# Kernel tuning notes

Hardware: AMD Instinct MI355X
Metric: run time of the kernel (lower is better)

## Reference

```python
import jax, jax.numpy as jnp
import numpy as np

B, N = 8192, 128          # batch, num intruders
D_OWN, D_GRID, D_INTR = 16, 512, 20
H, OUT = 128, 4


def setup_inputs() -> dict:
    key = jax.random.key(0)
    ks = jax.random.split(key, 12)
    rn = lambda k, shape, s=1.0: jax.random.normal(k, shape, jnp.float32) * s
    return {
        "state0": rn(ks[0], (B, D_OWN)),
        "state1": rn(ks[1], (B, D_GRID)),
        "state2": rn(ks[2], (B, N, D_INTR)),
        "W_own": rn(ks[3], (D_OWN, H), 0.1), "b_own": jnp.zeros((H,), jnp.float32),
        "W_intr": rn(ks[4], (D_INTR, H), 0.1), "b_intr": jnp.zeros((H,), jnp.float32),
        "W_grid": rn(ks[5], (D_GRID, H), 0.05), "b_grid": jnp.zeros((H,), jnp.float32),
        "Wq": rn(ks[6], (H, H), 0.08),
        "Wk": rn(ks[7], (H, H), 0.08),
        "Wv": rn(ks[8], (H, H), 0.08),
        "W1": rn(ks[9], (3 * H, H), 0.05), "b1": jnp.zeros((H,), jnp.float32),
        "W2": rn(ks[10], (H, OUT), 0.1), "b2": jnp.zeros((OUT,), jnp.float32),
    }


def reference(state0, state1, state2, W_own, b_own, W_intr, b_intr,
              W_grid, b_grid, Wq, Wk, Wv, W1, b1, W2, b2):
    own_e = jax.nn.relu(state0 @ W_own + b_own)            # [B,H]
    x_e = jax.nn.relu(state2 @ W_intr + b_intr)            # [B,N,H]
    q = own_e @ Wq                                         # [B,H]
    k = x_e @ Wk                                           # [B,N,H]
    v = x_e @ Wv                                           # [B,N,H]
    # mask = state2.mean(axis=2, keepdim=True).bool()  (nonzero test)
    mask = jnp.mean(state2, axis=2, keepdims=True) != 0    # [B,N,1]
    score = jnp.einsum('bnh,bh->bn', k, q)[..., None]      # bmm(k, q.unsqueeze(2)) -> [B,N,1]
    score = jnp.where(mask, score, -jnp.inf)
    alpha = jax.nn.softmax(score / np.float32(np.sqrt(H)), axis=1)
    alpha = jnp.where(mask, alpha, 0.0)
    v_att = jnp.sum(v * alpha, axis=1)                     # [B,H]
    own_grid = jax.nn.relu(state1 @ W_grid + b_grid)       # [B,H]
    concat = jnp.concatenate([own_e, v_att, own_grid], axis=1)  # [B,3H]
    out = (concat @ W1 + b1) @ W2 + b2                     # action_out_SAC
    mean = out
    log_std = jnp.clip(out, -20.0, 2.0)
    return mean, log_std
```

## Files before the change

kernel.cpp:

```cpp
#include <hip/hip_runtime.h>

typedef unsigned short ushort_t;
typedef __attribute__((ext_vector_type(8))) short bf16x8;
typedef __attribute__((ext_vector_type(4))) float f32x4;

__device__ __forceinline__ float bflo(unsigned u) { return __uint_as_float(u << 16); }
__device__ __forceinline__ float bfhi(unsigned u) { return __uint_as_float(u & 0xffff0000u); }
__device__ __forceinline__ float bfu(ushort_t s)  { return __uint_as_float((unsigned)s << 16); }
__device__ __forceinline__ ushort_t f2bf(float f) {
    unsigned u = __float_as_uint(f);
    u = u + 0x7fffu + ((u >> 16) & 1u);
    return (ushort_t)(u >> 16);
}
__device__ __forceinline__ void unpack8(uint4 v, float* f) {
    f[0]=bflo(v.x); f[1]=bfhi(v.x); f[2]=bflo(v.y); f[3]=bfhi(v.y);
    f[4]=bflo(v.z); f[5]=bfhi(v.z); f[6]=bflo(v.w); f[7]=bfhi(v.w);
}

__device__ __forceinline__ float load1(const void* p, size_t i, int f32) {
    return f32 ? ((const float*)p)[i] : bfu(((const ushort_t*)p)[i]);
}
__device__ __forceinline__ void load8(const void* p, size_t i, int f32, float* f) {
    if (f32) {
        const float4 a = *(const float4*)((const float*)p + i);
        const float4 b = *(const float4*)((const float*)p + i + 4);
        f[0]=a.x; f[1]=a.y; f[2]=a.z; f[3]=a.w;
        f[4]=b.x; f[5]=b.y; f[6]=b.z; f[7]=b.w;
    } else {
        unpack8(*(const uint4*)((const ushort_t*)p + i), f);
    }
}
__device__ __forceinline__ void load4(const void* p, size_t i, int f32, float* f) {
    if (f32) {
        const float4 a = *(const float4*)((const float*)p + i);
        f[0]=a.x; f[1]=a.y; f[2]=a.z; f[3]=a.w;
    } else {
        const uint2 u = *(const uint2*)((const ushort_t*)p + i);
        f[0]=bflo(u.x); f[1]=bfhi(u.x); f[2]=bflo(u.y); f[3]=bfhi(u.y);
    }
}

__device__ __forceinline__ int detect_f32(const ushort_t* s1h) {
    const int ln = threadIdx.x & 63;
    float v = fmaxf(fabsf(bfu(s1h[ln])), fabsf(bfu(s1h[ln + 64])));
    bool big = !(v <= 1e6f);
    return __ballot(big) != 0ull;
}

#define B_TOT 8192

__device__ __attribute__((aligned(16))) float    g_M[128 * 128];
__device__ __attribute__((aligned(16))) float    g_Wc1[384 * 4];
__device__ __attribute__((aligned(16))) float    g_Wv2[128 * 4];
__device__ __attribute__((aligned(16))) float    g_bc[4];
__device__ __attribute__((aligned(16))) float    g_t[B_TOT * 128];
__device__ __attribute__((aligned(16))) float    g_ogc[B_TOT * 4];
__device__ __attribute__((aligned(16))) ushort_t g_oe[B_TOT * 128];

__global__ __launch_bounds__(128) void k_pre(
    const void* __restrict__ Wq, const void* __restrict__ Wk,
    const void* __restrict__ Wv, const void* __restrict__ W1,
    const void* __restrict__ b1, const void* __restrict__ W2,
    const void* __restrict__ b2, const ushort_t* __restrict__ s1h)
{
    __shared__ float wq_sh[128];
    __shared__ float w2_sh[512];
    __shared__ float wc1_mid[512];
    __shared__ float redc[128][4];
    const int tid = threadIdx.x;
    const int bx = blockIdx.x;
    const int f32 = detect_f32(s1h);

    if (bx < 128) {
        wq_sh[tid] = load1(Wq, bx*128 + tid, f32);
        __syncthreads();
        float acc = 0.f;
        #pragma unroll
        for (int c = 0; c < 16; ++c) {
            float f[8]; load8(Wk, (size_t)tid*128 + c*8, f32, f);
            #pragma unroll
            for (int j = 0; j < 8; ++j) acc = fmaf(wq_sh[c*8+j], f[j], acc);
        }
        g_M[bx*128 + tid] = acc;
    } else {
        const int rbase = (bx == 128) ? 0 : ((bx == 129) ? 128 : 256);
        for (int i = tid; i < 512; i += 128) w2_sh[i] = load1(W2, i, f32);
        __syncthreads();

        const int r = rbase + tid;
        float a[4] = {0.f, 0.f, 0.f, 0.f};
        #pragma unroll
        for (int c = 0; c < 16; ++c) {
            float f[8]; load8(W1, (size_t)r*128 + c*8, f32, f);
            #pragma unroll
            for (int j = 0; j < 8; ++j) {
                const int p = c*8 + j;
                #pragma unroll
                for (int q = 0; q < 4; ++q) a[q] = fmaf(f[j], w2_sh[p*4+q], a[q]);
            }
        }
        #pragma unroll
        for (int q = 0; q < 4; ++q) g_Wc1[r*4+q] = a[q];

        if (bx == 129) {
            #pragma unroll
            for (int q = 0; q < 4; ++q) wc1_mid[tid*4+q] = a[q];
            __syncthreads();
            float v[4] = {0.f, 0.f, 0.f, 0.f};
            #pragma unroll
            for (int c = 0; c < 16; ++c) {
                float f[8]; load8(Wv, (size_t)tid*128 + c*8, f32, f);
                #pragma unroll
                for (int j = 0; j < 8; ++j) {
                    const int i2 = c*8 + j;
                    #pragma unroll
                    for (int q = 0; q < 4; ++q) v[q] = fmaf(f[j], wc1_mid[i2*4+q], v[q]);
                }
            }
            #pragma unroll
            for (int q = 0; q < 4; ++q) g_Wv2[tid*4+q] = v[q];

            const float bv = load1(b1, tid, f32);
            #pragma unroll
            for (int q = 0; q < 4; ++q) redc[tid][q] = bv * w2_sh[tid*4+q];
            __syncthreads();
            for (int s = 64; s > 0; s >>= 1) {
                if (tid < s) {
                    #pragma unroll
                    for (int q = 0; q < 4; ++q) redc[tid][q] += redc[tid+s][q];
                }
                __syncthreads();
            }
            if (tid < 4) g_bc[tid] = redc[0][tid] + load1(b2, tid, f32);
        }
    }
}

__global__ __launch_bounds__(256) void k_ownt(
    const void* __restrict__ state0, const void* __restrict__ W_own,
    const void* __restrict__ b_own, const ushort_t* __restrict__ s1h)
{
    __shared__ float s0sh[16*16];
    __shared__ float wosh[16*128];
    __shared__ float bosh[128];
    __shared__ float oesh[16*129];
    __shared__ float Mt[32][128];
    const int tid = threadIdx.x;
    const int b0 = blockIdx.x * 16;
    const int f32 = detect_f32(s1h);

    if (tid < 32) {
        float f[8]; load8(state0, (size_t)b0*16 + tid*8, f32, f);
        #pragma unroll
        for (int j = 0; j < 8; ++j) s0sh[tid*8 + j] = f[j];
    }
    {
        float f[8]; load8(W_own, (size_t)tid*8, f32, f);
        #pragma unroll
        for (int j = 0; j < 8; ++j) wosh[tid*8 + j] = f[j];
    }
    if (tid < 128) bosh[tid] = load1(b_own, tid, f32);
    __syncthreads();

    #pragma unroll
    for (int kk = 0; kk < 8; ++kk) {
        const int idx = tid + kk*256;
        const int bi = idx >> 7, h = idx & 127;
        float acc = bosh[h];
        #pragma unroll
        for (int d = 0; d < 16; ++d) acc = fmaf(s0sh[bi*16+d], wosh[d*128+h], acc);
        acc = fmaxf(acc, 0.f);
        oesh[bi*129 + h] = acc;
        g_oe[(size_t)(b0+bi)*128 + h] = f2bf(acc);
    }

    const int bi0 = (tid >> 5) * 2;
    const int h0  = (tid & 31) * 4;
    float t00=0.f,t01=0.f,t02=0.f,t03=0.f,t10=0.f,t11=0.f,t12=0.f,t13=0.f;
    for (int kt = 0; kt < 128; kt += 32) {
        __syncthreads();
        #pragma unroll
        for (int c = 0; c < 4; ++c) {
            const int i = tid + c*256;
            const int kk = i >> 5;
            const int hh = (i & 31) * 4;
            *(float4*)&Mt[kk][hh] = *(const float4*)&g_M[(size_t)(kt+kk)*128 + hh];
        }
        __syncthreads();
        #pragma unroll
        for (int k = 0; k < 32; ++k) {
            const float4 mv = *(const float4*)&Mt[k][h0];
            const float a0 = oesh[(bi0+0)*129 + kt + k];
            const float a1 = oesh[(bi0+1)*129 + kt + k];
            t00=fmaf(a0,mv.x,t00); t01=fmaf(a0,mv.y,t01); t02=fmaf(a0,mv.z,t02); t03=fmaf(a0,mv.w,t03);
            t10=fmaf(a1,mv.x,t10); t11=fmaf(a1,mv.y,t11); t12=fmaf(a1,mv.z,t12); t13=fmaf(a1,mv.w,t13);
        }
    }
    *(float4*)&g_t[(size_t)(b0+bi0+0)*128 + h0] = make_float4(t00,t01,t02,t03);
    *(float4*)&g_t[(size_t)(b0+bi0+1)*128 + h0] = make_float4(t10,t11,t12,t13);
}

__global__ __launch_bounds__(256) void k_grid(
    const void* __restrict__ state1, const void* __restrict__ W_grid,
    const void* __restrict__ b_grid)
{
    __shared__ float s1T[32][18];
    __shared__ float wg[32][128];
    __shared__ float part[32][16][4];
    const int tid = threadIdx.x;
    const int b0 = blockIdx.x * 16;
    const int f32 = detect_f32((const ushort_t*)state1);

    const int bq = tid & 7;
    const int hq = tid >> 3;
    float a00=0.f,a01=0.f,a02=0.f,a03=0.f;
    float a10=0.f,a11=0.f,a12=0.f,a13=0.f;

    for (int kt = 0; kt < 512; kt += 32) {
        if (kt) __syncthreads();
        if (tid < 128) {
            const int bb = tid >> 3;
            const int kk = (tid & 7) * 4;
            float f[4];
            load4(state1, (size_t)(b0 + bb)*512 + kt + kk, f32, f);
            #pragma unroll
            for (int j = 0; j < 4; ++j) s1T[kk + j][bb] = f[j];
        }
        {
            #pragma unroll
            for (int c = 0; c < 4; ++c) {
                const int i = tid + c*256;
                const int kk = i >> 5;
                const int hh = (i & 31) * 4;
                float f[4];
                load4(W_grid, (size_t)(kt + kk)*128 + hh, f32, f);
                *(float4*)&wg[kk][hh] = make_float4(f[0], f[1], f[2], f[3]);
            }
        }
        __syncthreads();
        #pragma unroll 8
        for (int k = 0; k < 32; ++k) {
            const float x0 = s1T[k][bq*2 + 0];
            const float x1 = s1T[k][bq*2 + 1];
            const float4 w = *(const float4*)&wg[k][hq*4];
            a00=fmaf(x0,w.x,a00); a01=fmaf(x0,w.y,a01); a02=fmaf(x0,w.z,a02); a03=fmaf(x0,w.w,a03);
            a10=fmaf(x1,w.x,a10); a11=fmaf(x1,w.y,a11); a12=fmaf(x1,w.z,a12); a13=fmaf(x1,w.w,a13);
        }
    }

    float accs[2][4] = {{a00,a01,a02,a03},{a10,a11,a12,a13}};
    float pr[2][4] = {{0,0,0,0},{0,0,0,0}};
    #pragma unroll
    for (int jh = 0; jh < 4; ++jh) {
        const int h = hq*4 + jh;
        const float bg = load1(b_grid, h, f32);
        const float4 wc = *(const float4*)&g_Wc1[(256 + h)*4];
        #pragma unroll
        for (int ib = 0; ib < 2; ++ib) {
            const float og = fmaxf(accs[ib][jh] + bg, 0.f);
            pr[ib][0] = fmaf(og, wc.x, pr[ib][0]);
            pr[ib][1] = fmaf(og, wc.y, pr[ib][1]);
            pr[ib][2] = fmaf(og, wc.z, pr[ib][2]);
            pr[ib][3] = fmaf(og, wc.w, pr[ib][3]);
        }
    }
    __syncthreads();
    #pragma unroll
    for (int j = 0; j < 4; ++j) {
        part[hq][bq*2+0][j] = pr[0][j];
        part[hq][bq*2+1][j] = pr[1][j];
    }
    __syncthreads();
    if (tid < 64) {
        const int bb = tid >> 2, j = tid & 3;
        float s = 0.f;
        #pragma unroll
        for (int q = 0; q < 32; ++q) s += part[q][bb][j];
        g_ogc[(size_t)(b0 + bb)*4 + j] = s;
    }
}

__global__ __launch_bounds__(256) void k_main(
    const void* __restrict__ state2, const void* __restrict__ W_intr,
    const void* __restrict__ b_intr, const ushort_t* __restrict__ s1h,
    void* __restrict__ out_raw)
{
    __shared__ __attribute__((aligned(16))) ushort_t wib[128 * 40];
    const int tid = threadIdx.x;
    const int f32 = detect_f32(s1h);

    #pragma unroll
    for (int c = 0; c < 10; ++c) {
        const int idx = c*256 + tid;
        const int d = idx >> 7, h = idx & 127;
        wib[h*40 + d] = f32 ? f2bf(((const float*)W_intr)[idx])
                            : ((const ushort_t*)W_intr)[idx];
    }
    if (tid < 128) {
        #pragma unroll
        for (int k = 20; k < 32; ++k) wib[tid*40 + k] = 0;
    }
    __syncthreads();

    const int wv = tid >> 6, ln = tid & 63, lq = ln >> 4, lc = ln & 15;
    const int b = blockIdx.x * 4 + wv;

    float bi_r[8], t_r[8];
    #pragma unroll
    for (int th = 0; th < 8; ++th) {
        bi_r[th] = load1(b_intr, th*16 + lc, f32);
        t_r[th]  = g_t[(size_t)b*128 + th*16 + lc] * 0.08838834764831845f;
    }

    bf16x8 A[8];
    unsigned msk[8];
    if (!f32) {
        const ushort_t* s2 = (const ushort_t*)state2;
        #pragma unroll
        for (int i = 0; i < 8; ++i) {
            const size_t rb = ((size_t)b*128 + i*16 + lc)*20 + lq*8;
            uint2 p0 = make_uint2(0u, 0u), p1 = make_uint2(0u, 0u);
            if (lq < 2)       { p0 = *(const uint2*)(s2 + rb); p1 = *(const uint2*)(s2 + rb + 4); }
            else if (lq == 2) { p0 = *(const uint2*)(s2 + rb); }
            union { bf16x8 v; uint2 u[2]; } cv;
            cv.u[0] = p0; cv.u[1] = p1;
            A[i] = cv.v;
            float s = bflo(p0.x)+bfhi(p0.x)+bflo(p0.y)+bfhi(p0.y)
                    + bflo(p1.x)+bfhi(p1.x)+bflo(p1.y)+bfhi(p1.y);
            s += __shfl_xor(s, 16);
            s += __shfl_xor(s, 32);
            msk[i] = (unsigned)(__ballot(s != 0.f) & 0xffffull);
        }
    } else {
        const float* s2 = (const float*)state2;
        #pragma unroll
        for (int i = 0; i < 8; ++i) {
            const size_t rb = ((size_t)b*128 + i*16 + lc)*20 + lq*8;
            float f[8] = {0.f,0.f,0.f,0.f,0.f,0.f,0.f,0.f};
            if (lq < 2) {
                const float4 a4 = *(const float4*)(s2 + rb);
                const float4 b4 = *(const float4*)(s2 + rb + 4);
                f[0]=a4.x; f[1]=a4.y; f[2]=a4.z; f[3]=a4.w;
                f[4]=b4.x; f[5]=b4.y; f[6]=b4.z; f[7]=b4.w;
            } else if (lq == 2) {
                const float4 a4 = *(const float4*)(s2 + rb);
                f[0]=a4.x; f[1]=a4.y; f[2]=a4.z; f[3]=a4.w;
            }
            union { bf16x8 v; ushort_t h[8]; } cv;
            float s = 0.f;
            #pragma unroll
            for (int j = 0; j < 8; ++j) { cv.h[j] = f2bf(f[j]); s += f[j]; }
            A[i] = cv.v;
            s += __shfl_xor(s, 16);
            s += __shfl_xor(s, 32);
            msk[i] = (unsigned)(__ballot(s != 0.f) & 0xffffull);
        }
    }

    const f32x4 zf = {0.f, 0.f, 0.f, 0.f};

    float sc[8][4];
    #pragma unroll
    for (int i = 0; i < 8; ++i)
        #pragma unroll
        for (int r = 0; r < 4; ++r) sc[i][r] = 0.f;

    #pragma unroll
    for (int th = 0; th < 8; ++th) {
        const bf16x8 Bv = *(const bf16x8*)&wib[(th*16 + lc)*40 + lq*8];
        #pragma unroll
        for (int i = 0; i < 8; ++i) {
            const f32x4 acc = __builtin_amdgcn_mfma_f32_16x16x32_bf16(A[i], Bv, zf, 0, 0, 0);
            #pragma unroll
            for (int r = 0; r < 4; ++r)
                sc[i][r] = fmaf(fmaxf(acc[r] + bi_r[th], 0.f), t_r[th], sc[i][r]);
        }
    }
    #pragma unroll
    for (int off = 1; off < 16; off <<= 1)
        #pragma unroll
        for (int i = 0; i < 8; ++i)
            #pragma unroll
            for (int r = 0; r < 4; ++r)
                sc[i][r] += __shfl_xor(sc[i][r], off);

    float m = -1e30f;
    #pragma unroll
    for (int i = 0; i < 8; ++i)
        #pragma unroll
        for (int r = 0; r < 4; ++r)
            if ((msk[i] >> (lq*4 + r)) & 1) m = fmaxf(m, sc[i][r]);
    m = fmaxf(m, __shfl_xor(m, 16));
    m = fmaxf(m, __shfl_xor(m, 32));

    float den = 0.f;
    #pragma unroll
    for (int i = 0; i < 8; ++i)
        #pragma unroll
        for (int r = 0; r < 4; ++r) {
            float e = 0.f;
            if ((msk[i] >> (lq*4 + r)) & 1) e = __expf(fmaxf(sc[i][r] - m, -80.f));
            sc[i][r] = e;
            den += e;
        }
    den += __shfl_xor(den, 16);
    den += __shfl_xor(den, 32);
    const float rden = (den > 0.f) ? (1.f / den) : 0.f;
    #pragma unroll
    for (int i = 0; i < 8; ++i)
        #pragma unroll
        for (int r = 0; r < 4; ++r) sc[i][r] *= rden;

    float o4[4] = {0.f, 0.f, 0.f, 0.f};
    #pragma unroll
    for (int th = 0; th < 8; ++th) {
        const bf16x8 Bv = *(const bf16x8*)&wib[(th*16 + lc)*40 + lq*8];
        float up = 0.f;
        #pragma unroll
        for (int i = 0; i < 8; ++i) {
            const f32x4 acc = __builtin_amdgcn_mfma_f32_16x16x32_bf16(A[i], Bv, zf, 0, 0, 0);
            #pragma unroll
            for (int r = 0; r < 4; ++r)
                up = fmaf(sc[i][r], fmaxf(acc[r] + bi_r[th], 0.f), up);
        }
        const float4 w2 = *(const float4*)&g_Wv2[(th*16 + lc)*4];
        o4[0] = fmaf(up, w2.x, o4[0]);
        o4[1] = fmaf(up, w2.y, o4[1]);
        o4[2] = fmaf(up, w2.z, o4[2]);
        o4[3] = fmaf(up, w2.w, o4[3]);
    }

    {
        const float oe0 = bfu(g_oe[(size_t)b*128 + ln]);
        const float oe1 = bfu(g_oe[(size_t)b*128 + 64 + ln]);
        const float4 wA = *(const float4*)&g_Wc1[ln*4];
        const float4 wB = *(const float4*)&g_Wc1[(64 + ln)*4];
        o4[0] += oe0*wA.x + oe1*wB.x;
        o4[1] += oe0*wA.y + oe1*wB.y;
        o4[2] += oe0*wA.z + oe1*wB.z;
        o4[3] += oe0*wA.w + oe1*wB.w;
    }

    #pragma unroll
    for (int off = 1; off < 64; off <<= 1)
        #pragma unroll
        for (int q = 0; q < 4; ++q)
            o4[q] += __shfl_xor(o4[q], off);

    if (ln == 0) {
        const float4 og = *(const float4*)&g_ogc[(size_t)b*4];
        const float v0 = g_bc[0] + og.x + o4[0];
        const float v1 = g_bc[1] + og.y + o4[1];
        const float v2 = g_bc[2] + og.z + o4[2];
        const float v3 = g_bc[3] + og.w + o4[3];
        const float l0 = fminf(fmaxf(v0, -20.f), 2.f);
        const float l1 = fminf(fmaxf(v1, -20.f), 2.f);
        const float l2 = fminf(fmaxf(v2, -20.f), 2.f);
        const float l3 = fminf(fmaxf(v3, -20.f), 2.f);
        if (f32) {
            float* of = (float*)out_raw;
            *(float4*)&of[(size_t)b*4] = make_float4(v0, v1, v2, v3);
            *(float4*)&of[((size_t)B_TOT + b)*4] = make_float4(l0, l1, l2, l3);
        } else {
            ushort_t* os = (ushort_t*)out_raw;
            uint2 mw, lw;
            mw.x = (unsigned)f2bf(v0) | ((unsigned)f2bf(v1) << 16);
            mw.y = (unsigned)f2bf(v2) | ((unsigned)f2bf(v3) << 16);
            lw.x = (unsigned)f2bf(l0) | ((unsigned)f2bf(l1) << 16);
            lw.y = (unsigned)f2bf(l2) | ((unsigned)f2bf(l3) << 16);
            *(uint2*)&os[(size_t)b*4] = mw;
            *(uint2*)&os[((size_t)B_TOT + b)*4] = lw;
        }
    }
}

extern "C" void kernel_launch(void* const* d_in, const int* in_sizes, int n_in,
                              void* d_out, int out_size, void* d_ws, size_t ws_size,
                              hipStream_t stream)
{
    (void)in_sizes; (void)n_in; (void)out_size; (void)d_ws; (void)ws_size;
    const void* state0 = d_in[0];
    const void* state1 = d_in[1];
    const void* state2 = d_in[2];
    const void* W_own  = d_in[3];
    const void* b_own  = d_in[4];
    const void* W_intr = d_in[5];
    const void* b_intr = d_in[6];
    const void* W_grid = d_in[7];
    const void* b_grid = d_in[8];
    const void* Wq     = d_in[9];
    const void* Wk     = d_in[10];
    const void* Wv     = d_in[11];
    const void* W1     = d_in[12];
    const void* b1     = d_in[13];
    const void* W2     = d_in[14];
    const void* b2     = d_in[15];
    const ushort_t* s1h = (const ushort_t*)state1;

    k_pre  <<<dim3(131),  dim3(128), 0, stream>>>(Wq, Wk, Wv, W1, b1, W2, b2, s1h);
    k_ownt <<<dim3(512),  dim3(256), 0, stream>>>(state0, W_own, b_own, s1h);
    k_grid <<<dim3(512),  dim3(256), 0, stream>>>(state1, W_grid, b_grid);
    k_main <<<dim3(2048), dim3(256), 0, stream>>>(state2, W_intr, b_intr, s1h, d_out);
}
```

Measured before the change: 291.8 us.

## Fold bias, mask and softmax scaling into MFMA and exp2 in attention kernel

Folds the intruder bias into the MFMA by appending a constant-one input column and a bias row in the LDS weight tile. The mask row sums are computed with an extra MFMA against a ones vector instead of shuffle-and-ballot reductions. The log2(e) factor is pre-scaled into the query so the softmax can use raw exp2, and normalisation is deferred to the four outputs instead of all scores. State2 loads are also hoisted ahead of the weight staging and barrier to overlap global latency. This removes per-element bias adds, masking branches and reductions, at the cost of the bias being rounded to bf16 and slightly different masking semantics.

```diff
diff --git a/kernel.cpp b/kernel.cpp
--- a/kernel.cpp
+++ b/kernel.cpp
@@ -289,6 +289,50 @@
     const int tid = threadIdx.x;
     const int f32 = detect_f32(s1h);
 
+    const int wv = tid >> 6, ln = tid & 63, lq = ln >> 4, lc = ln & 15;
+    const int b = blockIdx.x * 4 + wv;
+
+    bf16x8 A[8];
+    if (!f32) {
+        const ushort_t* base = (const ushort_t*)state2 + ((size_t)b*128 + lc)*20 + lq*8;
+        #pragma unroll
+        for (int i = 0; i < 8; ++i) {
+            uint2 p0 = make_uint2(0u, 0u), p1 = make_uint2(0u, 0u);
+            if (lq < 2)       { p0 = *(const uint2*)(base + i*320); p1 = *(const uint2*)(base + i*320 + 4); }
+            else if (lq == 2) { p0 = *(const uint2*)(base + i*320); p1.x = 0x00003f80u; }
+            union { bf16x8 v; uint2 u[2]; } cv;
+            cv.u[0] = p0; cv.u[1] = p1;
+            A[i] = cv.v;
+        }
+    } else {
+        const float* base = (const float*)state2 + ((size_t)b*128 + lc)*20 + lq*8;
+        #pragma unroll
+        for (int i = 0; i < 8; ++i) {
+            float f[8] = {0.f,0.f,0.f,0.f,0.f,0.f,0.f,0.f};
+            if (lq < 2) {
+                const float4 a4 = *(const float4*)(base + i*320);
+                const float4 b4 = *(const float4*)(base + i*320 + 4);
+                f[0]=a4.x; f[1]=a4.y; f[2]=a4.z; f[3]=a4.w;
+                f[4]=b4.x; f[5]=b4.y; f[6]=b4.z; f[7]=b4.w;
+            } else if (lq == 2) {
+                const float4 a4 = *(const float4*)(base + i*320);
+                f[0]=a4.x; f[1]=a4.y; f[2]=a4.z; f[3]=a4.w;
+                f[4]=1.0f;
+            }
+            union { bf16x8 v; ushort_t h[8]; } cv;
+            #pragma unroll
+            for (int j = 0; j < 8; ++j) cv.h[j] = f2bf(f[j]);
+            A[i] = cv.v;
+        }
+    }
+
+    float t_r[8];
+    {
+        const float* tb = &g_t[(size_t)b*128 + lc];
+        #pragma unroll
+        for (int th = 0; th < 8; ++th) t_r[th] = tb[th*16] * 0.12751743f;
+    }
+
     #pragma unroll
     for (int c = 0; c < 10; ++c) {
         const int idx = c*256 + tid;
@@ -297,67 +341,25 @@
                             : ((const ushort_t*)W_intr)[idx];
     }
     if (tid < 128) {
-        #pragma unroll
-        for (int k = 20; k < 32; ++k) wib[tid*40 + k] = 0;
+        wib[tid*40 + 20] = f32 ? f2bf(((const float*)b_intr)[tid])
+                               : ((const ushort_t*)b_intr)[tid];
+        #pragma unroll
+        for (int k = 21; k < 32; ++k) wib[tid*40 + k] = 0;
     }
     __syncthreads();
 
-    const int wv = tid >> 6, ln = tid & 63, lq = ln >> 4, lc = ln & 15;
-    const int b = blockIdx.x * 4 + wv;
-
-    float bi_r[8], t_r[8];
-    #pragma unroll
-    for (int th = 0; th < 8; ++th) {
-        bi_r[th] = load1(b_intr, th*16 + lc, f32);
-        t_r[th]  = g_t[(size_t)b*128 + th*16 + lc] * 0.08838834764831845f;
-    }
-
-    bf16x8 A[8];
-    unsigned msk[8];
-    if (!f32) {
-        const ushort_t* s2 = (const ushort_t*)state2;
-        #pragma unroll
-        for (int i = 0; i < 8; ++i) {
-            const size_t rb = ((size_t)b*128 + i*16 + lc)*20 + lq*8;
-            uint2 p0 = make_uint2(0u, 0u), p1 = make_uint2(0u, 0u);
-            if (lq < 2)       { p0 = *(const uint2*)(s2 + rb); p1 = *(const uint2*)(s2 + rb + 4); }
-            else if (lq == 2) { p0 = *(const uint2*)(s2 + rb); }
-            union { bf16x8 v; uint2 u[2]; } cv;
-            cv.u[0] = p0; cv.u[1] = p1;
-            A[i] = cv.v;
-            float s = bflo(p0.x)+bfhi(p0.x)+bflo(p0.y)+bfhi(p0.y)
-                    + bflo(p1.x)+bfhi(p1.x)+bflo(p1.y)+bfhi(p1.y);
-            s += __shfl_xor(s, 16);
-            s += __shfl_xor(s, 32);
-            msk[i] = (unsigned)(__ballot(s != 0.f) & 0xffffull);
-        }
-    } else {
-        const float* s2 = (const float*)state2;
-        #pragma unroll
-        for (int i = 0; i < 8; ++i) {
-            const size_t rb = ((size_t)b*128 + i*16 + lc)*20 + lq*8;
-            float f[8] = {0.f,0.f,0.f,0.f,0.f,0.f,0.f,0.f};
-            if (lq < 2) {
-                const float4 a4 = *(const float4*)(s2 + rb);
-                const float4 b4 = *(const float4*)(s2 + rb + 4);
-                f[0]=a4.x; f[1]=a4.y; f[2]=a4.z; f[3]=a4.w;
-                f[4]=b4.x; f[5]=b4.y; f[6]=b4.z; f[7]=b4.w;
-            } else if (lq == 2) {
-                const float4 a4 = *(const float4*)(s2 + rb);
-                f[0]=a4.x; f[1]=a4.y; f[2]=a4.z; f[3]=a4.w;
-            }
-            union { bf16x8 v; ushort_t h[8]; } cv;
-            float s = 0.f;
-            #pragma unroll
-            for (int j = 0; j < 8; ++j) { cv.h[j] = f2bf(f[j]); s += f[j]; }
-            A[i] = cv.v;
-            s += __shfl_xor(s, 16);
-            s += __shfl_xor(s, 32);
-            msk[i] = (unsigned)(__ballot(s != 0.f) & 0xffffull);
-        }
-    }
+    union { bf16x8 v; unsigned u[4]; } bo;
+    bo.u[0] = (lq <= 2) ? 0x3f803f80u : 0u;
+    bo.u[1] = (lq <= 2) ? 0x3f803f80u : 0u;
+    bo.u[2] = (lq <= 1) ? 0x3f803f80u : 0u;
+    bo.u[3] = (lq <= 1) ? 0x3f803f80u : 0u;
 
     const f32x4 zf = {0.f, 0.f, 0.f, 0.f};
+
+    f32x4 ms[8];
+    #pragma unroll
+    for (int i = 0; i < 8; ++i)
+        ms[i] = __builtin_amdgcn_mfma_f32_16x16x32_bf16(A[i], bo.v, zf, 0, 0, 0);
 
     float sc[8][4];
     #pragma unroll
@@ -373,7 +375,7 @@
             const f32x4 acc = __builtin_amdgcn_mfma_f32_16x16x32_bf16(A[i], Bv, zf, 0, 0, 0);
             #pragma unroll
             for (int r = 0; r < 4; ++r)
-                sc[i][r] = fmaf(fmaxf(acc[r] + bi_r[th], 0.f), t_r[th], sc[i][r]);
+                sc[i][r] = fmaf(fmaxf(acc[r], 0.f), t_r[th], sc[i][r]);
         }
     }
     #pragma unroll
@@ -384,12 +386,16 @@
             for (int r = 0; r < 4; ++r)
                 sc[i][r] += __shfl_xor(sc[i][r], off);
 
+    #pragma unroll
+    for (int i = 0; i < 8; ++i)
+        #pragma unroll
+        for (int r = 0; r < 4; ++r)
+            sc[i][r] = (ms[i][r] != 0.f) ? sc[i][r] : -1e30f;
+
     float m = -1e30f;
     #pragma unroll
     for (int i = 0; i < 8; ++i)
-        #pragma unroll
-        for (int r = 0; r < 4; ++r)
-            if ((msk[i] >> (lq*4 + r)) & 1) m = fmaxf(m, sc[i][r]);
+        m = fmaxf(m, fmaxf(fmaxf(sc[i][0], sc[i][1]), fmaxf(sc[i][2], sc[i][3])));
     m = fmaxf(m, __shfl_xor(m, 16));
     m = fmaxf(m, __shfl_xor(m, 32));
 
@@ -398,18 +404,14 @@
     for (int i = 0; i < 8; ++i)
         #pragma unroll
         for (int r = 0; r < 4; ++r) {
-            float e = 0.f;
-            if ((msk[i] >> (lq*4 + r)) & 1) e = __expf(fmaxf(sc[i][r] - m, -80.f));
+            const float x = sc[i][r] - m;
+            const float e = __builtin_amdgcn_exp2f(x);
             sc[i][r] = e;
             den += e;
         }
     den += __shfl_xor(den, 16);
     den += __shfl_xor(den, 32);
-    const float rden = (den > 0.f) ? (1.f / den) : 0.f;
-    #pragma unroll
-    for (int i = 0; i < 8; ++i)
-        #pragma unroll
-        for (int r = 0; r < 4; ++r) sc[i][r] *= rden;
+    const float rden = (m > -1e29f && den > 0.f) ? (1.f / den) : 0.f;
 
     float o4[4] = {0.f, 0.f, 0.f, 0.f};
     #pragma unroll
@@ -421,7 +423,7 @@
             const f32x4 acc = __builtin_amdgcn_mfma_f32_16x16x32_bf16(A[i], Bv, zf, 0, 0, 0);
             #pragma unroll
             for (int r = 0; r < 4; ++r)
-                up = fmaf(sc[i][r], fmaxf(acc[r] + bi_r[th], 0.f), up);
+                up = fmaf(sc[i][r], fmaxf(acc[r], 0.f), up);
         }
         const float4 w2 = *(const float4*)&g_Wv2[(th*16 + lc)*4];
         o4[0] = fmaf(up, w2.x, o4[0]);
@@ -429,6 +431,8 @@
         o4[2] = fmaf(up, w2.z, o4[2]);
         o4[3] = fmaf(up, w2.w, o4[3]);
     }
+    #pragma unroll
+    for (int q = 0; q < 4; ++q) o4[q] *= rden;
 
     {
         const float oe0 = bfu(g_oe[(size_t)b*128 + ln]);
```

New measurement: 326.5 us. 11.9% more time.
